# Kernel tuning notes

Measured on AMD Instinct MI355X. Metric: run time of the kernel, lower is better.

## Reference

```python
import jax, jax.numpy as jnp
import numpy as np

B, N, L, S = 512, 10020, 20, 10
H = (N - L) // S + 1  # 1001, hidden_remainder == 0 for these dims
INV_SQRT6 = float(1.0 / np.sqrt(6.0))  # e3nn TensorProduct 1o x 1o -> 1e, irrep_normalization='none' (raw wigner-3j)


def q_mult(q1, q2):
    w1, x1, y1, z1 = q1[..., 0], q1[..., 1], q1[..., 2], q1[..., 3]
    w2, x2, y2, z2 = q2[..., 0], q2[..., 1], q2[..., 2], q2[..., 3]
    w = w1 * w2 - x1 * x2 - y1 * y2 - z1 * z2
    x = w1 * x2 + x1 * w2 + y1 * z2 - z1 * y2
    y = w1 * y2 + y1 * w2 + z1 * x2 - x1 * z2
    z = w1 * z2 + z1 * w2 + x1 * y2 - y1 * x2
    return jnp.stack((w, x, y, z), -1)


def qv_mult(q1, v2):
    q2 = jnp.concatenate([jnp.zeros(v2.shape[:-1] + (1,), v2.dtype), v2], -1)
    q1c = q1 * jnp.asarray([1.0, -1.0, -1.0, -1.0], q1.dtype)
    return q_mult(q_mult(q1, q2), q1c)[..., 1:]


def setup_inputs() -> dict:
    key = jax.random.key(0)
    ks = jax.random.split(key, 5)
    return {
        "x": jax.random.normal(ks[0], (B, N, 3), jnp.float32),
        "W_enc": jax.random.normal(ks[1], (L, H, 3), jnp.float32),
        "W_dec": jax.random.normal(ks[2], (3, H, L), jnp.float32),
        "angles_polar": jax.random.normal(ks[3], (H * L, 1), jnp.float32),
        "scaling": jax.random.normal(ks[4], (H * L, 1), jnp.float32),
    }


def reference(x, W_enc, W_dec, angles_polar, scaling):
    batch, n = x.shape[0], x.shape[1]
    # ---- encode: as_strided gather -> (b, L, H, 3), st[b,l,h] = x[b, l + S*h]
    idx = jnp.arange(L)[:, None] + S * jnp.arange(H)[None, :]  # (L,H)
    st = x[:, idx]  # (b,L,H,3)
    emb = jnp.einsum('bijk,ijl->bjlk', st, W_enc)  # (b,H,3,3): P, I1, I2
    P, I1, I2 = emb[:, :, 0], emb[:, :, 1], emb[:, :, 2]

    def _unit(v):
        nrm = jnp.linalg.norm(v, axis=-1, keepdims=True)
        return v / jnp.where(nrm == 0, jnp.asarray(1.0, v.dtype), nrm)

    p1, p2 = _unit(I1 - P), _unit(I2 - P)
    # ---- decode
    p12 = jnp.cross(p1, p2) * INV_SQRT6  # o3 TensorProduct, 'uuu', norm='none'
    stacked = jnp.stack([p1, p2, p12], axis=1)  # (b,3,H,3)
    rot_axes = jnp.einsum('bijk,ijl->bjlk', stacked, W_dec).reshape(-1, 3)  # (b*H*L,3)
    q = jnp.concatenate([
        jnp.tile(jnp.cos(angles_polar), (batch, 1)),
        jnp.tile(jnp.sin(angles_polar), (batch, 1)) * rot_axes,
    ], -1)  # (b*H*L,4)
    v1 = jnp.repeat(p1.reshape(-1, 3), L, axis=0)  # repeat_interleave over (b*H)
    v3 = qv_mult(q, v1).reshape(batch, H, L, 3)
    # ---- contribution_beads (static structure), vectorized
    idcs = jnp.arange(1, n + 1, dtype=jnp.float32)
    started = jnp.ceil(idcs / S).astype(jnp.int32)
    started = started.at[n - L:].set(started[n - L])  # partial_n == n here
    ended = jnp.maximum(jnp.ceil((idcs - L) / S), 0.0).astype(jnp.int32)
    hgrid = jnp.arange(H)
    contribution = ((hgrid[None, :] >= ended[:, None]) & (hgrid[None, :] < started[:, None])).astype(x.dtype)  # (n,H)
    # ---- normalized_weights: nw[i,h] = contribution[i,h] * W_enc[i - S*h, h, 0] if 0 <= i-S*h < L
    shift = jnp.arange(n)[:, None] - S * hgrid[None, :]  # (n,H)
    valid = (shift >= 0) & (shift < L)
    gathered = jnp.take_along_axis(W_enc[:, :, 0], jnp.clip(shift, 0, L - 1), axis=0)  # (n,H)
    nw = jnp.where(valid, contribution * gathered, jnp.asarray(0.0, x.dtype))
    nw = nw / nw.sum(axis=1, keepdims=True)
    # ---- fused weighted scatter-add reconstruction
    atom_idx = S * hgrid[:, None] + jnp.arange(L)[None, :]  # (H,L), atom = S*h + l
    scale_g = scaling[atom_idx.reshape(-1)].reshape(H, L, 1)  # scaling[S*h + l]
    nw_g = nw[atom_idx, hgrid[:, None]]  # (H,L)
    rec = (scale_g[None] * v3 + P[:, :, None, :]) * nw_g[None, :, :, None]  # (b,H,L,3)
    reconstructed = jnp.zeros((batch, n, 3), x.dtype).at[:, atom_idx.reshape(-1)].add(rec.reshape(batch, -1, 3))
    return (reconstructed, P, p1, p2, st, rot_axes, nw, contribution)
```

## Files before the change

kernel.cpp:

```cpp
#include <hip/hip_runtime.h>
#include <math.h>

#define BB 512
#define NN 10020
#define LL 20
#define SS 10
#define HH 1001
#define HL (HH*LL)
#define INV_SQRT6 0.40824829046386296f
#define TPB 256
#define NT 4

#define SZ_REC  (BB*NN*3)
#define SZ_BH3  (BB*HH*3)
#define SZ_ST   (BB*LL*HH*3)
#define SZ_ROT  (BB*HH*LL*3)
#define SZ_NH   (NN*HH)
#define O_REC   0
#define O_P     (O_REC + SZ_REC)
#define O_P1    (O_P   + SZ_BH3)
#define O_P2    (O_P1  + SZ_BH3)
#define O_ST    (O_P2  + SZ_BH3)
#define O_ROT   (O_ST  + SZ_ST)
#define O_NW    (O_ROT + SZ_ROT)
#define O_CT    (O_NW  + SZ_NH)

__global__ void k_tab(const float* __restrict__ ang, const float* __restrict__ W_enc,
                      float2* __restrict__ cs, float* __restrict__ gt) {
    int t = blockIdx.x * blockDim.x + threadIdx.x;
    if (t >= HL) return;
    float a = ang[t];
    cs[t] = make_float2(cosf(a), sinf(a));
    int h = t / LL, l = t - LL * (t / LL);
    int n = SS * h + l;
    int ended = (n >= LL) ? (n - SS) / SS : 0;
    int hhi = n / SS; if (hhi > HH - 1) hhi = HH - 1;
    float denom = 0.f;
    for (int hp = ended; hp <= hhi; ++hp)
        denom += W_enc[(size_t)((n - SS * hp) * HH + hp) * 3];
    gt[t] = W_enc[(size_t)(l * HH + h) * 3] / denom;
}

__global__ void k_band(const float* __restrict__ W_enc,
                       float* __restrict__ nw, float* __restrict__ ct) {
    int i = blockIdx.x * blockDim.x + threadIdx.x;
    if (i >= NN) return;
    int ended = (i >= LL) ? (i - SS) / SS : 0;
    int hhi = i / SS; if (hhi > HH - 1) hhi = HH - 1;
    float denom = 0.f;
    for (int hp = ended; hp <= hhi; ++hp)
        denom += W_enc[(size_t)((i - SS * hp) * HH + hp) * 3];
    size_t row = (size_t)i * HH;
    for (int h = ended; h <= hhi; ++h) {
        ct[row + h] = 1.0f;
        nw[row + h] = W_enc[(size_t)((i - SS * h) * HH + h) * 3] / denom;
    }
}

__global__ void __launch_bounds__(TPB) k_main(
    const float*  __restrict__ x,       const float* __restrict__ W_enc,
    const float*  __restrict__ W_dec,   const float* __restrict__ ang,
    const float2* __restrict__ cs_tab,  const float* __restrict__ g_tab,
    const float*  __restrict__ scaling, const float* __restrict__ nw,
    float* __restrict__ recon, float* __restrict__ Pout,
    float* __restrict__ p1out, float* __restrict__ p2out,
    float* __restrict__ stout, float* __restrict__ rotout) {

    __shared__ float xs[(SS*TPB + SS) * 3];
    __shared__ float rb[(SS*TPB + SS) * 3];

    int tile = blockIdx.x & (NT - 1);
    int b    = blockIdx.x >> 2;
    int h0   = tile * TPB;
    int cnt  = HH - h0; if (cnt > TPB) cnt = TPB;
    int t    = threadIdx.x;
    int a0   = SS * h0;
    int nf   = (SS * cnt + SS) * 3;

    const float* xsrc = x + ((size_t)b * NN + a0) * 3;
    for (int j = t; j < nf; j += TPB) xs[j] = xsrc[j];
    __syncthreads();

    for (int i = 0; i < LL; ++i) {
        float* dst = stout + (((size_t)b * LL + i) * HH + h0) * 3;
        for (int j = t; j < cnt * 3; j += TPB) {
            int hh = j / 3, k = j - 3 * hh;
            dst[j] = xs[(SS * hh + i) * 3 + k];
        }
    }

    int h = h0 + t;
    float Px=0,Py=0,Pz=0, p1x=0,p1y=0,p1z=0, p2x=0,p2y=0,p2z=0;
    float ra[3 * LL];

    if (t < cnt) {
        float e00=0,e01=0,e02=0, e10=0,e11=0,e12=0, e20=0,e21=0,e22=0;
        const float* xl = xs + (size_t)SS * t * 3;
#pragma unroll
        for (int i = 0; i < LL; ++i) {
            float v0 = xl[i*3+0], v1 = xl[i*3+1], v2 = xl[i*3+2];
            const float* we = W_enc + ((size_t)i * HH + h) * 3;
            float w0 = we[0], w1 = we[1], w2 = we[2];
            e00 = fmaf(v0, w0, e00); e01 = fmaf(v1, w0, e01); e02 = fmaf(v2, w0, e02);
            e10 = fmaf(v0, w1, e10); e11 = fmaf(v1, w1, e11); e12 = fmaf(v2, w1, e12);
            e20 = fmaf(v0, w2, e20); e21 = fmaf(v1, w2, e21); e22 = fmaf(v2, w2, e22);
        }
        Px = e00; Py = e01; Pz = e02;
        float d1x = e10-Px, d1y = e11-Py, d1z = e12-Pz;
        float d2x = e20-Px, d2y = e21-Py, d2z = e22-Pz;
        float n1 = sqrtf(d1x*d1x + d1y*d1y + d1z*d1z); if (n1 == 0.f) n1 = 1.f;
        float n2 = sqrtf(d2x*d2x + d2y*d2y + d2z*d2z); if (n2 == 0.f) n2 = 1.f;
        p1x = d1x/n1; p1y = d1y/n1; p1z = d1z/n1;
        p2x = d2x/n2; p2y = d2y/n2; p2z = d2z/n2;
        float cx = (p1y*p2z - p1z*p2y) * INV_SQRT6;
        float cy = (p1z*p2x - p1x*p2z) * INV_SQRT6;
        float cz = (p1x*p2y - p1y*p2x) * INV_SQRT6;

        size_t bh = (size_t)b * HH + h;
        Pout [bh*3+0]=Px;  Pout [bh*3+1]=Py;  Pout [bh*3+2]=Pz;
        p1out[bh*3+0]=p1x; p1out[bh*3+1]=p1y; p1out[bh*3+2]=p1z;
        p2out[bh*3+0]=p2x; p2out[bh*3+1]=p2y; p2out[bh*3+2]=p2z;

        const float* wd0 = W_dec + (size_t)h * LL;
        const float* wd1 = wd0 + (size_t)HH * LL;
        const float* wd2 = wd1 + (size_t)HH * LL;
#pragma unroll
        for (int l = 0; l < LL; ++l) {
            float w0 = wd0[l], w1 = wd1[l], w2 = wd2[l];
            ra[l*3+0] = p1x*w0 + p2x*w1 + cx*w2;
            ra[l*3+1] = p1y*w0 + p2y*w1 + cy*w2;
            ra[l*3+2] = p1z*w0 + p2z*w1 + cz*w2;
        }
        float4* ro4 = (float4*)(rotout + bh * (size_t)(LL*3));
#pragma unroll
        for (int q = 0; q < (3*LL)/4; ++q)
            ro4[q] = make_float4(ra[4*q+0], ra[4*q+1], ra[4*q+2], ra[4*q+3]);
    }

    auto contrib = [&](int l, float* c3) {
        float r0 = ra[l*3+0], r1 = ra[l*3+1], r2 = ra[l*3+2];
        float ca, sa, g;
        if (cs_tab) {
            float2 c2 = cs_tab[h*LL + l]; ca = c2.x; sa = c2.y;
            g = g_tab[h*LL + l];
        } else {
            float a = ang[h*LL + l]; ca = cosf(a); sa = sinf(a);
            g = nw[(size_t)(SS*h + l) * HH + h];
        }
        float qx = sa*r0, qy = sa*r1, qz = sa*r2;
        float tt = ca*ca - (qx*qx + qy*qy + qz*qz);
        float rv = qx*p1x + qy*p1y + qz*p1z;
        float axv = qy*p1z - qz*p1y;
        float ayv = qz*p1x - qx*p1z;
        float azv = qx*p1y - qy*p1x;
        float sc = scaling[SS*h + l];
        c3[0] = (sc * (tt*p1x + 2.f*(rv*qx + ca*axv)) + Px) * g;
        c3[1] = (sc * (tt*p1y + 2.f*(rv*qy + ca*ayv)) + Py) * g;
        c3[2] = (sc * (tt*p1z + 2.f*(rv*qz + ca*azv)) + Pz) * g;
    };

    if (t < cnt) {
        for (int l = 0; l < SS; ++l) {
            float c3[3]; contrib(l, c3);
            rb[30*t + 3*l + 0] = c3[0];
            rb[30*t + 3*l + 1] = c3[1];
            rb[30*t + 3*l + 2] = c3[2];
        }
        if (t == cnt - 1) {
            for (int l = SS; l < LL; ++l) {
                float c3[3]; contrib(l, c3);
                rb[30*t + 3*l + 0] = c3[0];
                rb[30*t + 3*l + 1] = c3[1];
                rb[30*t + 3*l + 2] = c3[2];
            }
        }
    }
    __syncthreads();
    if (t < cnt - 1) {
        for (int l = SS; l < LL; ++l) {
            float c3[3]; contrib(l, c3);
            rb[30*t + 3*l + 0] += c3[0];
            rb[30*t + 3*l + 1] += c3[1];
            rb[30*t + 3*l + 2] += c3[2];
        }
    }
    __syncthreads();

    float* rdst = recon + ((size_t)b * NN + a0) * 3;
    int interiorEnd = 30 * cnt;
    for (int j = 30 + t; j < interiorEnd; j += TPB) rdst[j] = rb[j];
    if (t < 30) atomicAdd(rdst + t, rb[t]);
    if (t >= 64 && t < 94) {
        int j = interiorEnd + (t - 64);
        atomicAdd(rdst + j, rb[j]);
    }
}

extern "C" void kernel_launch(void* const* d_in, const int* in_sizes, int n_in,
                              void* d_out, int out_size, void* d_ws, size_t ws_size,
                              hipStream_t stream) {
    const float* x       = (const float*)d_in[0];
    const float* W_enc   = (const float*)d_in[1];
    const float* W_dec   = (const float*)d_in[2];
    const float* ang     = (const float*)d_in[3];
    const float* scaling = (const float*)d_in[4];
    float* out = (float*)d_out;

    float2* cs = nullptr; float* gt = nullptr;
    size_t need = (size_t)HL * (sizeof(float2) + sizeof(float));
    if (ws_size >= need) {
        cs = (float2*)d_ws;
        gt = (float*)(cs + HL);
    }

    hipMemsetAsync(out + O_REC, 0, (size_t)SZ_REC * sizeof(float), stream);
    hipMemsetAsync(out + O_NW, 0, (size_t)(2 * SZ_NH) * sizeof(float), stream);

    if (cs) k_tab<<<(HL + 255)/256, 256, 0, stream>>>(ang, W_enc, cs, gt);
    k_band<<<(NN + 255)/256, 256, 0, stream>>>(W_enc, out + O_NW, out + O_CT);

    k_main<<<BB * NT, TPB, 0, stream>>>(
        x, W_enc, W_dec, ang, cs, gt, scaling, out + O_NW,
        out + O_REC, out + O_P, out + O_P1, out + O_P2, out + O_ST, out + O_ROT);
}
```

Baseline: 584.9 us.

## Alias reduction buffer onto input LDS, recompute rot axes, raise occupancy

The reduction buffer now reuses the shared-memory input tile, with an added barrier, which halves LDS use per block. The 60-float per-thread rot-axis array is dropped; rot-axes are written in chunks of four and recomputed from W_dec inside the contribution lambda. Launch bounds now request 4 blocks per CU, and the input tile is loaded with float4. The aim is lower register and LDS pressure for higher occupancy on a memory-bound kernel, paid for with extra W_dec reloads and some recomputation.

```diff
diff --git a/kernel.cpp b/kernel.cpp
--- a/kernel.cpp
+++ b/kernel.cpp
@@ -57,7 +57,7 @@
     }
 }
 
-__global__ void __launch_bounds__(TPB) k_main(
+__global__ void __launch_bounds__(TPB, 4) k_main(
     const float*  __restrict__ x,       const float* __restrict__ W_enc,
     const float*  __restrict__ W_dec,   const float* __restrict__ ang,
     const float2* __restrict__ cs_tab,  const float* __restrict__ g_tab,
@@ -67,7 +67,7 @@
     float* __restrict__ stout, float* __restrict__ rotout) {
 
     __shared__ float xs[(SS*TPB + SS) * 3];
-    __shared__ float rb[(SS*TPB + SS) * 3];
+    float* rb = xs;
 
     int tile = blockIdx.x & (NT - 1);
     int b    = blockIdx.x >> 2;
@@ -78,7 +78,13 @@
     int nf   = (SS * cnt + SS) * 3;
 
     const float* xsrc = x + ((size_t)b * NN + a0) * 3;
-    for (int j = t; j < nf; j += TPB) xs[j] = xsrc[j];
+    {
+        const float4* xs4 = (const float4*)xsrc;
+        float4* xl4 = (float4*)xs;
+        int nf4 = nf >> 2;
+        for (int j = t; j < nf4; j += TPB) xl4[j] = xs4[j];
+        for (int j = (nf4 << 2) + t; j < nf; j += TPB) xs[j] = xsrc[j];
+    }
     __syncthreads();
 
     for (int i = 0; i < LL; ++i) {
@@ -91,7 +97,8 @@
 
     int h = h0 + t;
     float Px=0,Py=0,Pz=0, p1x=0,p1y=0,p1z=0, p2x=0,p2y=0,p2z=0;
-    float ra[3 * LL];
+    float cx=0, cy=0, cz=0;
+    const float* wd0 = nullptr; const float* wd1 = nullptr; const float* wd2 = nullptr;
 
     if (t < cnt) {
         float e00=0,e01=0,e02=0, e10=0,e11=0,e12=0, e20=0,e21=0,e22=0;
@@ -112,33 +119,43 @@
         float n2 = sqrtf(d2x*d2x + d2y*d2y + d2z*d2z); if (n2 == 0.f) n2 = 1.f;
         p1x = d1x/n1; p1y = d1y/n1; p1z = d1z/n1;
         p2x = d2x/n2; p2y = d2y/n2; p2z = d2z/n2;
-        float cx = (p1y*p2z - p1z*p2y) * INV_SQRT6;
-        float cy = (p1z*p2x - p1x*p2z) * INV_SQRT6;
-        float cz = (p1x*p2y - p1y*p2x) * INV_SQRT6;
+        cx = (p1y*p2z - p1z*p2y) * INV_SQRT6;
+        cy = (p1z*p2x - p1x*p2z) * INV_SQRT6;
+        cz = (p1x*p2y - p1y*p2x) * INV_SQRT6;
 
         size_t bh = (size_t)b * HH + h;
         Pout [bh*3+0]=Px;  Pout [bh*3+1]=Py;  Pout [bh*3+2]=Pz;
         p1out[bh*3+0]=p1x; p1out[bh*3+1]=p1y; p1out[bh*3+2]=p1z;
         p2out[bh*3+0]=p2x; p2out[bh*3+1]=p2y; p2out[bh*3+2]=p2z;
 
-        const float* wd0 = W_dec + (size_t)h * LL;
-        const float* wd1 = wd0 + (size_t)HH * LL;
-        const float* wd2 = wd1 + (size_t)HH * LL;
-#pragma unroll
-        for (int l = 0; l < LL; ++l) {
-            float w0 = wd0[l], w1 = wd1[l], w2 = wd2[l];
-            ra[l*3+0] = p1x*w0 + p2x*w1 + cx*w2;
-            ra[l*3+1] = p1y*w0 + p2y*w1 + cy*w2;
-            ra[l*3+2] = p1z*w0 + p2z*w1 + cz*w2;
-        }
+        wd0 = W_dec + (size_t)h * LL;
+        wd1 = wd0 + (size_t)HH * LL;
+        wd2 = wd1 + (size_t)HH * LL;
+
         float4* ro4 = (float4*)(rotout + bh * (size_t)(LL*3));
 #pragma unroll
-        for (int q = 0; q < (3*LL)/4; ++q)
-            ro4[q] = make_float4(ra[4*q+0], ra[4*q+1], ra[4*q+2], ra[4*q+3]);
-    }
+        for (int lq = 0; lq < LL/4; ++lq) {
+            float v[12];
+#pragma unroll
+            for (int u = 0; u < 4; ++u) {
+                int l = 4*lq + u;
+                float w0 = wd0[l], w1 = wd1[l], w2 = wd2[l];
+                v[3*u+0] = fmaf(p1x, w0, fmaf(p2x, w1, cx*w2));
+                v[3*u+1] = fmaf(p1y, w0, fmaf(p2y, w1, cy*w2));
+                v[3*u+2] = fmaf(p1z, w0, fmaf(p2z, w1, cz*w2));
+            }
+            ro4[3*lq+0] = make_float4(v[0], v[1], v[2],  v[3]);
+            ro4[3*lq+1] = make_float4(v[4], v[5], v[6],  v[7]);
+            ro4[3*lq+2] = make_float4(v[8], v[9], v[10], v[11]);
+        }
+    }
+    __syncthreads();
 
     auto contrib = [&](int l, float* c3) {
-        float r0 = ra[l*3+0], r1 = ra[l*3+1], r2 = ra[l*3+2];
+        float w0 = wd0[l], w1 = wd1[l], w2 = wd2[l];
+        float r0 = fmaf(p1x, w0, fmaf(p2x, w1, cx*w2));
+        float r1 = fmaf(p1y, w0, fmaf(p2y, w1, cy*w2));
+        float r2 = fmaf(p1z, w0, fmaf(p2z, w1, cz*w2));
         float ca, sa, g;
         if (cs_tab) {
             float2 c2 = cs_tab[h*LL + l]; ca = c2.x; sa = c2.y;
```

Result: slower. 634.7 us (+8.5%).

## Vectorize global stores, pack per-atom tables as coalesced float4, alias shared buffers

Applied to the files above, without the earlier changes.

Precomputes packed float4 tables in l-major layout: cos, sin, scaling*weight and weight, plus the three W_dec values per (h,l). Adjacent threads then read contiguous float4s instead of strided scalars. The x tile load, st gather stores and interior recon stores move to float4 where alignment allows, with scalar prologue and epilogue handling. The reconstruction buffer now reuses the x shared-memory array, which halves LDS use to raise occupancy at the cost of an extra barrier. The per-thread maths is also rewritten into fma chains.

```diff
diff --git a/kernel.cpp b/kernel.cpp
--- a/kernel.cpp
+++ b/kernel.cpp
@@ -26,19 +26,24 @@
 #define O_CT    (O_NW  + SZ_NH)
 
 __global__ void k_tab(const float* __restrict__ ang, const float* __restrict__ W_enc,
-                      float2* __restrict__ cs, float* __restrict__ gt) {
+                      const float* __restrict__ W_dec, const float* __restrict__ scaling,
+                      float4* __restrict__ tab4, float4* __restrict__ wd4) {
     int t = blockIdx.x * blockDim.x + threadIdx.x;
     if (t >= HL) return;
-    float a = ang[t];
-    cs[t] = make_float2(cosf(a), sinf(a));
-    int h = t / LL, l = t - LL * (t / LL);
+    int l = t / HH, h = t - HH * l;
     int n = SS * h + l;
     int ended = (n >= LL) ? (n - SS) / SS : 0;
     int hhi = n / SS; if (hhi > HH - 1) hhi = HH - 1;
     float denom = 0.f;
     for (int hp = ended; hp <= hhi; ++hp)
         denom += W_enc[(size_t)((n - SS * hp) * HH + hp) * 3];
-    gt[t] = W_enc[(size_t)(l * HH + h) * 3] / denom;
+    float g = W_enc[(size_t)(l * HH + h) * 3] / denom;
+    float a = ang[h * LL + l];
+    float sc = scaling[n];
+    tab4[t] = make_float4(cosf(a), sinf(a), sc * g, g);
+    wd4[t]  = make_float4(W_dec[(size_t)h * LL + l],
+                          W_dec[(size_t)(HH * LL) + (size_t)h * LL + l],
+                          W_dec[(size_t)(2 * HH * LL) + (size_t)h * LL + l], 0.f);
 }
 
 __global__ void k_band(const float* __restrict__ W_enc,
@@ -60,14 +65,14 @@
 __global__ void __launch_bounds__(TPB) k_main(
     const float*  __restrict__ x,       const float* __restrict__ W_enc,
     const float*  __restrict__ W_dec,   const float* __restrict__ ang,
-    const float2* __restrict__ cs_tab,  const float* __restrict__ g_tab,
+    const float4* __restrict__ tab4,    const float4* __restrict__ wd4,
     const float*  __restrict__ scaling, const float* __restrict__ nw,
     float* __restrict__ recon, float* __restrict__ Pout,
     float* __restrict__ p1out, float* __restrict__ p2out,
     float* __restrict__ stout, float* __restrict__ rotout) {
 
     __shared__ float xs[(SS*TPB + SS) * 3];
-    __shared__ float rb[(SS*TPB + SS) * 3];
+    float* rb = xs;
 
     int tile = blockIdx.x & (NT - 1);
     int b    = blockIdx.x >> 2;
@@ -78,14 +83,43 @@
     int nf   = (SS * cnt + SS) * 3;
 
     const float* xsrc = x + ((size_t)b * NN + a0) * 3;
-    for (int j = t; j < nf; j += TPB) xs[j] = xsrc[j];
-    __syncthreads();
-
-    for (int i = 0; i < LL; ++i) {
-        float* dst = stout + (((size_t)b * LL + i) * HH + h0) * 3;
-        for (int j = t; j < cnt * 3; j += TPB) {
-            int hh = j / 3, k = j - 3 * hh;
-            dst[j] = xs[(SS * hh + i) * 3 + k];
+    {
+        const float4* xs4 = (const float4*)xsrc;
+        float4* xl4 = (float4*)xs;
+        int nf4 = nf >> 2;
+        for (int j = t; j < nf4; j += TPB) xl4[j] = xs4[j];
+        for (int j = (nf4 << 2) + t; j < nf; j += TPB) xs[j] = xsrc[j];
+    }
+    __syncthreads();
+
+    {
+        int M = cnt * 3;
+        for (int i = 0; i < LL; ++i) {
+            float* dst = stout + (((size_t)b * LL + i) * HH + h0) * 3;
+            int pre = i & 3;
+            if (t < pre) {
+                int hh = t / 3, k = t - 3 * hh;
+                dst[t] = xs[(SS * hh + i) * 3 + k];
+            }
+            int nv4 = (M - pre) >> 2;
+            float4* d4 = (float4*)(dst + pre);
+            for (int q = t; q < nv4; q += TPB) {
+                int j = pre + 4 * q;
+                int h0i = j / 3, k0 = j - 3 * h0i;
+                float4 v;
+                v.x = xs[(SS * h0i + i) * 3 + k0];
+                int j1 = j + 1; int h1i = j1 / 3, k1 = j1 - 3 * h1i;
+                v.y = xs[(SS * h1i + i) * 3 + k1];
+                int j2 = j + 2; int h2i = j2 / 3, k2 = j2 - 3 * h2i;
+                v.z = xs[(SS * h2i + i) * 3 + k2];
+                int j3 = j + 3; int h3i = j3 / 3, k3 = j3 - 3 * h3i;
+                v.w = xs[(SS * h3i + i) * 3 + k3];
+                d4[q] = v;
+            }
+            for (int j = pre + (nv4 << 2) + t; j < M; j += TPB) {
+                int hh = j / 3, k = j - 3 * hh;
+                dst[j] = xs[(SS * hh + i) * 3 + k];
+            }
         }
     }
 
@@ -121,31 +155,43 @@
         p1out[bh*3+0]=p1x; p1out[bh*3+1]=p1y; p1out[bh*3+2]=p1z;
         p2out[bh*3+0]=p2x; p2out[bh*3+1]=p2y; p2out[bh*3+2]=p2z;
 
-        const float* wd0 = W_dec + (size_t)h * LL;
-        const float* wd1 = wd0 + (size_t)HH * LL;
-        const float* wd2 = wd1 + (size_t)HH * LL;
-#pragma unroll
-        for (int l = 0; l < LL; ++l) {
-            float w0 = wd0[l], w1 = wd1[l], w2 = wd2[l];
-            ra[l*3+0] = p1x*w0 + p2x*w1 + cx*w2;
-            ra[l*3+1] = p1y*w0 + p2y*w1 + cy*w2;
-            ra[l*3+2] = p1z*w0 + p2z*w1 + cz*w2;
+        if (wd4) {
+#pragma unroll
+            for (int l = 0; l < LL; ++l) {
+                float4 w = wd4[l * HH + h];
+                ra[l*3+0] = fmaf(p1x, w.x, fmaf(p2x, w.y, cx*w.z));
+                ra[l*3+1] = fmaf(p1y, w.x, fmaf(p2y, w.y, cy*w.z));
+                ra[l*3+2] = fmaf(p1z, w.x, fmaf(p2z, w.y, cz*w.z));
+            }
+        } else {
+            const float* wd0 = W_dec + (size_t)h * LL;
+            const float* wd1 = wd0 + (size_t)HH * LL;
+            const float* wd2 = wd1 + (size_t)HH * LL;
+#pragma unroll
+            for (int l = 0; l < LL; ++l) {
+                float w0 = wd0[l], w1 = wd1[l], w2 = wd2[l];
+                ra[l*3+0] = fmaf(p1x, w0, fmaf(p2x, w1, cx*w2));
+                ra[l*3+1] = fmaf(p1y, w0, fmaf(p2y, w1, cy*w2));
+                ra[l*3+2] = fmaf(p1z, w0, fmaf(p2z, w1, cz*w2));
+            }
         }
         float4* ro4 = (float4*)(rotout + bh * (size_t)(LL*3));
 #pragma unroll
         for (int q = 0; q < (3*LL)/4; ++q)
             ro4[q] = make_float4(ra[4*q+0], ra[4*q+1], ra[4*q+2], ra[4*q+3]);
     }
+    __syncthreads();
 
     auto contrib = [&](int l, float* c3) {
         float r0 = ra[l*3+0], r1 = ra[l*3+1], r2 = ra[l*3+2];
-        float ca, sa, g;
-        if (cs_tab) {
-            float2 c2 = cs_tab[h*LL + l]; ca = c2.x; sa = c2.y;
-            g = g_tab[h*LL + l];
+        float ca, sa, sg, g;
+        if (tab4) {
+            float4 tv = tab4[l * HH + h];
+            ca = tv.x; sa = tv.y; sg = tv.z; g = tv.w;
         } else {
             float a = ang[h*LL + l]; ca = cosf(a); sa = sinf(a);
             g = nw[(size_t)(SS*h + l) * HH + h];
+            sg = scaling[SS*h + l] * g;
         }
         float qx = sa*r0, qy = sa*r1, qz = sa*r2;
         float tt = ca*ca - (qx*qx + qy*qy + qz*qz);
@@ -153,10 +199,9 @@
         float axv = qy*p1z - qz*p1y;
         float ayv = qz*p1x - qx*p1z;
         float azv = qx*p1y - qy*p1x;
-        float sc = scaling[SS*h + l];
-        c3[0] = (sc * (tt*p1x + 2.f*(rv*qx + ca*axv)) + Px) * g;
-        c3[1] = (sc * (tt*p1y + 2.f*(rv*qy + ca*ayv)) + Py) * g;
-        c3[2] = (sc * (tt*p1z + 2.f*(rv*qz + ca*azv)) + Pz) * g;
+        c3[0] = fmaf(sg, fmaf(tt, p1x, 2.f*fmaf(rv, qx, ca*axv)), g*Px);
+        c3[1] = fmaf(sg, fmaf(tt, p1y, 2.f*fmaf(rv, qy, ca*ayv)), g*Py);
+        c3[2] = fmaf(sg, fmaf(tt, p1z, 2.f*fmaf(rv, qz, ca*azv)), g*Pz);
     };
 
     if (t < cnt) {
@@ -188,7 +233,14 @@
 
     float* rdst = recon + ((size_t)b * NN + a0) * 3;
     int interiorEnd = 30 * cnt;
-    for (int j = 30 + t; j < interiorEnd; j += TPB) rdst[j] = rb[j];
+    {
+        int ie4 = interiorEnd >> 2;
+        float4* r4 = (float4*)rdst;
+        for (int q = 8 + t; q < ie4; q += TPB)
+            r4[q] = make_float4(rb[4*q+0], rb[4*q+1], rb[4*q+2], rb[4*q+3]);
+        if (t < 2) rdst[30 + t] = rb[30 + t];
+        for (int j = (ie4 << 2) + t; j < interiorEnd; j += TPB) rdst[j] = rb[j];
+    }
     if (t < 30) atomicAdd(rdst + t, rb[t]);
     if (t >= 64 && t < 94) {
         int j = interiorEnd + (t - 64);
@@ -206,20 +258,20 @@
     const float* scaling = (const float*)d_in[4];
     float* out = (float*)d_out;
 
-    float2* cs = nullptr; float* gt = nullptr;
-    size_t need = (size_t)HL * (sizeof(float2) + sizeof(float));
+    float4* tab4 = nullptr; float4* wd4 = nullptr;
+    size_t need = (size_t)HL * sizeof(float4) * 2;
     if (ws_size >= need) {
-        cs = (float2*)d_ws;
-        gt = (float*)(cs + HL);
+        tab4 = (float4*)d_ws;
+        wd4  = tab4 + HL;
     }
 
     hipMemsetAsync(out + O_REC, 0, (size_t)SZ_REC * sizeof(float), stream);
     hipMemsetAsync(out + O_NW, 0, (size_t)(2 * SZ_NH) * sizeof(float), stream);
 
-    if (cs) k_tab<<<(HL + 255)/256, 256, 0, stream>>>(ang, W_enc, cs, gt);
+    if (tab4) k_tab<<<(HL + 255)/256, 256, 0, stream>>>(ang, W_enc, W_dec, scaling, tab4, wd4);
     k_band<<<(NN + 255)/256, 256, 0, stream>>>(W_enc, out + O_NW, out + O_CT);
 
     k_main<<<BB * NT, TPB, 0, stream>>>(
-        x, W_enc, W_dec, ang, cs, gt, scaling, out + O_NW,
+        x, W_enc, W_dec, ang, tab4, wd4, scaling, out + O_NW,
         out + O_REC, out + O_P, out + O_P1, out + O_P2, out + O_ST, out + O_ROT);
 }
```

Measured after the change: 523.6 us. 10.5% less time.
